# Kernel tuning notes

Measured on AMD Instinct MI355X. Metric: run time of the kernel, lower is better.

## Reference

```python
import jax, jax.numpy as jnp
import numpy as np

ALPHA = 0.2  # LeakyReLU negative slope
N = 1024     # num_particles
DIM = 3
F_IN = 2 * DIM   # 6
NH = 64          # n_hidden_features
H = 4            # n_heads
T = 12


def _gat_attend(feat, a_vec, slope):
    # feat: (..., N, K); a_vec: (..., 2K) split into source/dest halves
    k = feat.shape[-1]
    f_src = jnp.einsum('...nk,...k->...n', feat, a_vec[..., :k])
    f_dst = jnp.einsum('...nk,...k->...n', feat, a_vec[..., k:])
    e = jax.nn.leaky_relu(f_src[..., :, None] + f_dst[..., None, :], slope)
    attn = jax.nn.softmax(e, axis=-1)  # (..., N, N) dense particle attention
    return jnp.einsum('...ij,...jk->...ik', attn, feat)


def pat_layer(x, W_heads, a_heads, W_out, a_out):
    # x: (N, F_IN); W_heads: (H, F_IN, NH); a_heads: (H, 2*NH)
    # W_out: (H*NH, F_OUT); a_out: (2*F_OUT)
    hW = jnp.einsum('nf,hfk->hnk', x, W_heads)          # (H, N, NH)
    heads = jax.nn.elu(_gat_attend(hW, a_heads, ALPHA))  # (H, N, NH)
    x2 = heads.transpose(1, 0, 2).reshape(x.shape[0], -1)  # (N, H*NH) concat
    hW2 = x2 @ W_out                                     # (N, F_OUT)
    return _gat_attend(hW2, a_out, ALPHA)                # output head, no elu


def setup_inputs() -> dict:
    key = jax.random.key(0)
    ks = jax.random.split(key, 13)
    s = 0.1
    d = {'states': jax.random.normal(ks[0], (T, N, F_IN), jnp.float32)}
    names = ['Wx', 'ax', 'Wxo', 'axo', 'Wh', 'ah', 'Who', 'aho', 'Wy', 'ay', 'Wyo', 'ayo']
    shapes = [(H, F_IN, NH), (H, 2 * NH), (H * NH, F_IN), (2 * F_IN)] * 3
    for i, (nm, sh) in enumerate(zip(names, shapes)):
        sh = sh if isinstance(sh, tuple) else (sh,)
        d[nm] = s * jax.random.normal(ks[i + 1], sh, jnp.float32)
    return d


def reference(states, Wx, ax, Wxo, axo, Wh, ah, Who, aho, Wy, ay, Wyo, ayo):
    def step(h_prev, x_t):
        h_t = pat_layer(x_t, Wx, ax, Wxo, axo) + pat_layer(h_prev, Wh, ah, Who, aho)
        y_t = x_t + pat_layer(h_t, Wy, ay, Wyo, ayo)
        return h_t, y_t

    h0 = jnp.zeros((N, F_IN), states.dtype)
    _, ys = jax.lax.scan(step, h0, states)
    return ys  # (T, N, 2*dim)
```

## Files before the change

### kernel.cpp

```cpp
#include <hip/hip_runtime.h>
#include <hip/hip_bf16.h>

#define ALPHA 0.2f

typedef float v2f __attribute__((ext_vector_type(2)));
typedef short bf16x8 __attribute__((ext_vector_type(8)));
typedef float f32x4 __attribute__((ext_vector_type(4)));

__device__ __forceinline__ float wsum(float v){
  #pragma unroll
  for (int m = 1; m < 64; m <<= 1) v += __shfl_xor(v, m, 64);
  return v;
}
__device__ __forceinline__ float wmax(float v){
  #pragma unroll
  for (int m = 1; m < 64; m <<= 1) v = fmaxf(v, __shfl_xor(v, m, 64));
  return v;
}

__global__ void k_detect(const unsigned short* __restrict__ s, int n, int* __restrict__ flag){
  int i = blockIdx.x * 256 + threadIdx.x;
  if (i < n){
    unsigned short u = s[i];
    if ((u & 0x7F80u) == 0x7F80u) atomicOr(flag, 1);
  }
}

struct Ptr13 { const void* p[13]; };
__global__ void k_cvtAll(Ptr13 src, float* __restrict__ xs, float* __restrict__ wsW,
                         const int* __restrict__ flag){
  const int n = blockIdx.x * 256 + threadIdx.x;
  const int F = *flag;
  if (n < 73728){
    xs[n] = F ? ((const float*)src.p[0])[n]
              : __bfloat162float(((const __hip_bfloat16*)src.p[0])[n]);
    return;
  }
  const int m = n - 73728;
  if (m >= 10788) return;
  const int segend[12] = {1536,2048,3584,3596,5132,5644,7180,7192,8728,9240,10776,10788};
  const int dstoff[12] = {0,1536,2048,3584,3600,5136,5648,7184,7200,8736,9248,10784};
  int seg = 0;
  #pragma unroll
  for (int i = 0; i < 12; ++i) if (m >= segend[i]) seg = i + 1;
  const int local = m - (seg ? segend[seg - 1] : 0);
  float v;
  if (F) v = ((const float*)src.p[seg + 1])[local];
  else   v = __bfloat162float(((const __hip_bfloat16*)src.p[seg + 1])[local]);
  wsW[dstoff[seg] + local] = v;
}

__launch_bounds__(256)
__global__ void k_prepT(const float* __restrict__ X, const float* __restrict__ W,
                        const float* __restrict__ a,
                        __hip_bfloat16* __restrict__ Vt, float* __restrict__ fsd)
{
  __shared__ float WS[384];
  __shared__ float aS[128];
  __shared__ __align__(16) __hip_bfloat16 tileT[64 * 264];
  const int t = threadIdx.x;
  const int b = blockIdx.y;
  const int h = blockIdx.z;
  const int row0 = blockIdx.x * 256;
  const int row = row0 + t;
  for (int i = t; i < 384; i += 256) WS[i] = W[h * 384 + i];
  if (t < 128) aS[t] = a[h * 128 + t];
  __syncthreads();
  float x[6];
  const float* xp = X + ((size_t)b * 1024 + row) * 6;
  #pragma unroll
  for (int f = 0; f < 6; ++f) x[f] = xp[f];
  float fs = 0.f, fd = 0.f;
  for (int k = 0; k < 64; ++k){
    float v = 0.f;
    #pragma unroll
    for (int f = 0; f < 6; ++f) v += x[f] * WS[f * 64 + k];
    fs += v * aS[k]; fd += v * aS[64 + k];
    tileT[k * 264 + t] = __float2bfloat16(v);
  }
  fsd[(((size_t)b * 4 + h) * 2 + 0) * 1024 + row] = fs;
  fsd[(((size_t)b * 4 + h) * 2 + 1) * 1024 + row] = fd;
  __syncthreads();
  const int k = t >> 2, seg = t & 3;
  __hip_bfloat16* dst = Vt + (((size_t)b * 4 + h) * 64 + k) * 1032 + row0 + seg * 64;
  const __hip_bfloat16* src = tileT + k * 264 + seg * 64;
  #pragma unroll
  for (int i = 0; i < 8; ++i)
    ((uint4*)dst)[i] = ((const uint4*)src)[i];
}

__launch_bounds__(256)
__global__ void k_attM(const __hip_bfloat16* __restrict__ Vt, const float* __restrict__ fsd,
                       const float* __restrict__ Wout, const float* __restrict__ aout,
                       float* __restrict__ hW2part, float* __restrict__ f2part)
{
  const int h = blockIdx.x & 3;
  const int row0 = (blockIdx.x >> 2) * 64;
  const int b = blockIdx.y;
  const int t = threadIdx.x;
  const int wv = t >> 6, lane = t & 63;
  const int n = lane & 15, q = lane >> 4;
  const size_t bh = (size_t)b * 4 + h;

  __shared__ float dS[1024];
  __shared__ float WoS[384];
  __shared__ float aoS[12];
  __shared__ float redW[4];

  const float* fb = fsd + bh * 2048;
  float4 dv = *(const float4*)(fb + 1024 + t * 4);
  for (int i = t; i < 384; i += 256) WoS[i] = Wout[h * 384 + i];
  if (t < 12) aoS[t] = aout[t];
  *(float4*)&dS[t * 4] = dv;
  const float sW = fb[row0 + wv * 16 + n];
  float lm = fmaxf(fmaxf(dv.x, dv.y), fmaxf(dv.z, dv.w));
  lm = wmax(lm);
  if (lane == 0) redW[wv] = lm;
  __syncthreads();
  const float maxd = fmaxf(fmaxf(redW[0], redW[1]), fmaxf(redW[2], redW[3]));
  float mW = sW + maxd; mW = fmaxf(mW, ALPHA * mW);

  const __hip_bfloat16* vbase = Vt + (bh * 64 + n) * 1032 + q * 8;
  f32x4 acc[4];
  #pragma unroll
  for (int nt = 0; nt < 4; ++nt) acc[nt] = (f32x4){0.f, 0.f, 0.f, 0.f};
  float den = 0.f;

  for (int jt = 0; jt < 16; ++jt){
    bf16x8 b0[4], b1[4];
    #pragma unroll
    for (int nt = 0; nt < 4; ++nt){
      b0[nt] = *(const bf16x8*)(vbase + nt * 16512 + jt * 64);
      b1[nt] = *(const bf16x8*)(vbase + nt * 16512 + jt * 64 + 32);
    }
    const float* dp = &dS[jt * 64 + q * 8];
    float d0[8], d1[8];
    *(float4*)&d0[0] = *(const float4*)(dp);
    *(float4*)&d0[4] = *(const float4*)(dp + 4);
    *(float4*)&d1[0] = *(const float4*)(dp + 32);
    *(float4*)&d1[4] = *(const float4*)(dp + 36);
    bf16x8 a0, a1;
    #pragma unroll
    for (int i = 0; i < 8; ++i){
      float e0 = sW + d0[i]; e0 = fmaxf(e0, ALPHA * e0);
      __hip_bfloat16 w0 = __float2bfloat16(__expf(fminf(e0 - mW, 0.f)));
      a0[i] = __builtin_bit_cast(short, w0);
      den += __bfloat162float(w0);
      float e1 = sW + d1[i]; e1 = fmaxf(e1, ALPHA * e1);
      __hip_bfloat16 w1 = __float2bfloat16(__expf(fminf(e1 - mW, 0.f)));
      a1[i] = __builtin_bit_cast(short, w1);
      den += __bfloat162float(w1);
    }
    #pragma unroll
    for (int nt = 0; nt < 4; ++nt)
      acc[nt] = __builtin_amdgcn_mfma_f32_16x16x32_bf16(a0, b0[nt], acc[nt], 0, 0, 0);
    #pragma unroll
    for (int nt = 0; nt < 4; ++nt)
      acc[nt] = __builtin_amdgcn_mfma_f32_16x16x32_bf16(a1, b1[nt], acc[nt], 0, 0, 0);
  }
  den += __shfl_xor(den, 16, 64);
  den += __shfl_xor(den, 32, 64);

  float o[4][6];
  #pragma unroll
  for (int reg = 0; reg < 4; ++reg)
    #pragma unroll
    for (int f = 0; f < 6; ++f) o[reg][f] = 0.f;
  #pragma unroll
  for (int reg = 0; reg < 4; ++reg){
    const float dn = __shfl(den, q * 4 + reg, 64);
    #pragma unroll
    for (int nt = 0; nt < 4; ++nt){
      float v = acc[nt][reg] / dn;
      v = v > 0.f ? v : (__expf(v) - 1.f);
      #pragma unroll
      for (int f = 0; f < 6; ++f) o[reg][f] += v * WoS[(nt * 16 + n) * 6 + f];
    }
  }
  #pragma unroll
  for (int mm = 1; mm < 16; mm <<= 1)
    #pragma unroll
    for (int reg = 0; reg < 4; ++reg)
      #pragma unroll
      for (int f = 0; f < 6; ++f) o[reg][f] += __shfl_xor(o[reg][f], mm, 64);
  if (n == 0){
    #pragma unroll
    for (int reg = 0; reg < 4; ++reg){
      const int row = row0 + wv * 16 + q * 4 + reg;
      float* hp = hW2part + bh * 6144 + row * 6;
      float fs = 0.f, fd = 0.f;
      #pragma unroll
      for (int f = 0; f < 6; ++f){
        hp[f] = o[reg][f];
        fs += o[reg][f] * aoS[f]; fd += o[reg][f] * aoS[6 + f];
      }
      f2part[bh * 2048 + row]        = fs;
      f2part[bh * 2048 + 1024 + row] = fd;
    }
  }
}

__launch_bounds__(256)
__global__ void k_attP(const __hip_bfloat16* __restrict__ VtP, const float* __restrict__ fsd,
                       const float* __restrict__ Wout, const float* __restrict__ aout,
                       float* __restrict__ hW2part, float* __restrict__ f2part)
{
  const int h = blockIdx.x & 3;
  const int row0 = (blockIdx.x >> 2) * 16;
  const int t = threadIdx.x;
  const int wv = t >> 6, lane = t & 63;
  const int n = lane & 15, q = lane >> 4;

  __shared__ float dS[1024];
  __shared__ float WoS[384];
  __shared__ float aoS[12];
  __shared__ float redW[4];
  __shared__ float accS[4][16][65];
  __shared__ float denP[4][16];

  const float* fb = fsd + (size_t)h * 2048;
  float4 dv = *(const float4*)(fb + 1024 + t * 4);
  for (int i = t; i < 384; i += 256) WoS[i] = Wout[h * 384 + i];
  if (t < 12) aoS[t] = aout[t];
  *(float4*)&dS[t * 4] = dv;
  const float sW = fb[row0 + n];
  float lm = fmaxf(fmaxf(dv.x, dv.y), fmaxf(dv.z, dv.w));
  lm = wmax(lm);
  if (lane == 0) redW[wv] = lm;
  __syncthreads();
  const float maxd = fmaxf(fmaxf(redW[0], redW[1]), fmaxf(redW[2], redW[3]));
  float mW = sW + maxd; mW = fmaxf(mW, ALPHA * mW);

  const __hip_bfloat16* vbase = VtP + ((size_t)h * 64 + n) * 1024 + q * 8;
  f32x4 acc[4];
  #pragma unroll
  for (int nt = 0; nt < 4; ++nt) acc[nt] = (f32x4){0.f, 0.f, 0.f, 0.f};
  float den = 0.f;

  #pragma unroll
  for (int u = 0; u < 4; ++u){
    const int jt = wv * 4 + u;
    bf16x8 b0[4], b1[4];
    #pragma unroll
    for (int nt = 0; nt < 4; ++nt){
      b0[nt] = *(const bf16x8*)(vbase + nt * 16384 + jt * 64);
      b1[nt] = *(const bf16x8*)(vbase + nt * 16384 + jt * 64 + 32);
    }
    const float* dp = &dS[jt * 64 + q * 8];
    float d0[8], d1[8];
    *(float4*)&d0[0] = *(const float4*)(dp);
    *(float4*)&d0[4] = *(const float4*)(dp + 4);
    *(float4*)&d1[0] = *(const float4*)(dp + 32);
    *(float4*)&d1[4] = *(const float4*)(dp + 36);
    bf16x8 a0, a1;
    #pragma unroll
    for (int i = 0; i < 8; ++i){
      float e0 = sW + d0[i]; e0 = fmaxf(e0, ALPHA * e0);
      __hip_bfloat16 w0 = __float2bfloat16(__expf(fminf(e0 - mW, 0.f)));
      a0[i] = __builtin_bit_cast(short, w0);
      den += __bfloat162float(w0);
      float e1 = sW + d1[i]; e1 = fmaxf(e1, ALPHA * e1);
      __hip_bfloat16 w1 = __float2bfloat16(__expf(fminf(e1 - mW, 0.f)));
      a1[i] = __builtin_bit_cast(short, w1);
      den += __bfloat162float(w1);
    }
    #pragma unroll
    for (int nt = 0; nt < 4; ++nt)
      acc[nt] = __builtin_amdgcn_mfma_f32_16x16x32_bf16(a0, b0[nt], acc[nt], 0, 0, 0);
    #pragma unroll
    for (int nt = 0; nt < 4; ++nt)
      acc[nt] = __builtin_amdgcn_mfma_f32_16x16x32_bf16(a1, b1[nt], acc[nt], 0, 0, 0);
  }
  den += __shfl_xor(den, 16, 64);
  den += __shfl_xor(den, 32, 64);
  if (lane < 16) denP[wv][lane] = den;
  #pragma unroll
  for (int nt = 0; nt < 4; ++nt)
    #pragma unroll
    for (int reg = 0; reg < 4; ++reg)
      accS[wv][q * 4 + reg][nt * 16 + n] = acc[nt][reg];
  __syncthreads();

  const int r = t >> 4, kq = t & 15;
  const float dn = denP[0][r] + denP[1][r] + denP[2][r] + denP[3][r];
  float o[6] = {0.f,0.f,0.f,0.f,0.f,0.f};
  #pragma unroll
  for (int j4 = 0; j4 < 4; ++j4){
    const int k = kq * 4 + j4;
    float v = (accS[0][r][k] + accS[1][r][k] + accS[2][r][k] + accS[3][r][k]) / dn;
    v = v > 0.f ? v : (__expf(v) - 1.f);
    #pragma unroll
    for (int f = 0; f < 6; ++f) o[f] += v * WoS[k * 6 + f];
  }
  #pragma unroll
  for (int mm = 1; mm < 16; mm <<= 1)
    #pragma unroll
    for (int f = 0; f < 6; ++f) o[f] += __shfl_xor(o[f], mm, 64);
  if (kq == 0){
    const int row = row0 + r;
    float* hp = hW2part + (size_t)h * 6144 + row * 6;
    float fs = 0.f, fd = 0.f;
    #pragma unroll
    for (int f = 0; f < 6; ++f){
      hp[f] = o[f];
      fs += o[f] * aoS[f]; fd += o[f] * aoS[6 + f];
    }
    f2part[(size_t)h * 2048 + row]        = fs;
    f2part[(size_t)h * 2048 + 1024 + row] = fd;
  }
}

__launch_bounds__(256)
__global__ void k_attB(const float* __restrict__ hW2part, const float* __restrict__ f2part,
                       const float* __restrict__ Lx_t, float* __restrict__ h_t,
                       const float* __restrict__ Wh, const float* __restrict__ ah,
                       __hip_bfloat16* __restrict__ hWn, float* __restrict__ fn)
{
  const int t = threadIdx.x;
  const int row0 = blockIdx.x * 4;
  const int wv = t >> 6, lane = t & 63;
  __shared__ float featS[6144];
  __shared__ float dS[1024];
  __shared__ float sS[4];
  __shared__ float redW[4];
  __shared__ float htS[4][6];
  __shared__ float WnS[1536];
  __shared__ float anS[512];

  for (int i = t; i < 6144; i += 256)
    featS[i] = hW2part[i] + hW2part[6144 + i] + hW2part[12288 + i] + hW2part[18432 + i];
  for (int i = t; i < 1024; i += 256)
    dS[i] = f2part[1024 + i] + f2part[3072 + i] + f2part[5120 + i] + f2part[7168 + i];
  if (t < 4){
    const int r = row0 + t;
    sS[t] = f2part[r] + f2part[2048 + r] + f2part[4096 + r] + f2part[6144 + r];
  }
  for (int i = t; i < 1536; i += 256) WnS[i] = Wh[i];
  for (int i = t; i < 512;  i += 256) anS[i] = ah[i];
  __syncthreads();
  float lm = -1.0e30f;
  for (int i = t; i < 1024; i += 256) lm = fmaxf(lm, dS[i]);
  lm = wmax(lm);
  if (lane == 0) redW[wv] = lm;
  __syncthreads();
  const float maxd = fmaxf(fmaxf(redW[0], redW[1]), fmaxf(redW[2], redW[3]));
  {
    const int r = wv, row = row0 + r;
    const float s = sS[r];
    float m = s + maxd; m = m > 0.f ? m : ALPHA * m;
    float num[6] = {0.f,0.f,0.f,0.f,0.f,0.f};
    float den = 0.f;
    for (int j = lane; j < 1024; j += 64){
      float e = s + dS[j]; e = e > 0.f ? e : ALPHA * e;
      float w = __expf(fminf(e - m, 0.f));
      den += w;
      const float* fr = &featS[j * 6];
      #pragma unroll
      for (int f = 0; f < 6; ++f) num[f] += w * fr[f];
    }
    den = wsum(den);
    #pragma unroll
    for (int f = 0; f < 6; ++f) num[f] = wsum(num[f]);
    if (lane == 0){
      #pragma unroll
      for (int f = 0; f < 6; ++f){
        float hv = Lx_t[row * 6 + f] + num[f] / den;
        h_t[row * 6 + f] = hv;
        htS[r][f] = hv;
      }
    }
  }
  __syncthreads();
  {
    const int k = lane, rw = row0 + wv;
    float hv[6];
    #pragma unroll
    for (int f = 0; f < 6; ++f) hv[f] = htS[wv][f];
    #pragma unroll
    for (int h = 0; h < 4; ++h){
      float acc = 0.f;
      #pragma unroll
      for (int f = 0; f < 6; ++f) acc += hv[f] * WnS[(h * 6 + f) * 64 + k];
      hWn[((size_t)h * 64 + k) * 1024 + rw] = __float2bfloat16(acc);
      float ps = wsum(acc * anS[h * 128 + k]);
      float pd = wsum(acc * anS[h * 128 + 64 + k]);
      if (k == 0){
        fn[((size_t)h * 2 + 0) * 1024 + rw] = ps;
        fn[((size_t)h * 2 + 1) * 1024 + rw] = pd;
      }
    }
  }
}

template<int MODE>
__launch_bounds__(256)
__global__ void k_attO(const float* __restrict__ hW2part, const float* __restrict__ f2part,
                       const float* __restrict__ addsrc, float* __restrict__ outf,
                       void* __restrict__ outv, int outOff, const int* __restrict__ flag)
{
  const int b = blockIdx.y;
  const int row0 = blockIdx.x * 16;
  const int t = threadIdx.x;
  const int wv = t >> 6, lane = t & 63;
  __shared__ float featS[6144];
  __shared__ float dS[1024];
  __shared__ float sS[16];
  __shared__ float redW[4];

  const float* hp = hW2part + (size_t)b * 24576;
  for (int i = t; i < 6144; i += 256)
    featS[i] = hp[i] + hp[6144 + i] + hp[12288 + i] + hp[18432 + i];
  const float* fp = f2part + (size_t)b * 8192;
  for (int i = t; i < 1024; i += 256)
    dS[i] = fp[1024 + i] + fp[3072 + i] + fp[5120 + i] + fp[7168 + i];
  if (t < 16){
    const int r = row0 + t;
    sS[t] = fp[r] + fp[2048 + r] + fp[4096 + r] + fp[6144 + r];
  }
  __syncthreads();
  float lm = -1.0e30f;
  for (int i = t; i < 1024; i += 256) lm = fmaxf(lm, dS[i]);
  lm = wmax(lm);
  if (lane == 0) redW[wv] = lm;
  __syncthreads();
  const float maxd = fmaxf(fmaxf(redW[0], redW[1]), fmaxf(redW[2], redW[3]));

  const int r = t >> 4, jq = t & 15;
  const int row = row0 + r;
  const float s = sS[r];
  float m = s + maxd; m = m > 0.f ? m : ALPHA * m;
  float num[6] = {0.f,0.f,0.f,0.f,0.f,0.f};
  float den = 0.f;
  for (int j = jq; j < 1024; j += 16){
    float e = s + dS[j]; e = e > 0.f ? e : ALPHA * e;
    float w = __expf(fminf(e - m, 0.f));
    den += w;
    const float* fr = &featS[j * 6];
    #pragma unroll
    for (int f = 0; f < 6; ++f) num[f] += w * fr[f];
  }
  #pragma unroll
  for (int mm = 1; mm < 16; mm <<= 1){
    den += __shfl_xor(den, mm, 64);
    #pragma unroll
    for (int f = 0; f < 6; ++f) num[f] += __shfl_xor(num[f], mm, 64);
  }

  if (jq == 0){
    if (MODE == 0){
      float* dst = outf + ((size_t)b * 1024 + row) * 6;
      #pragma unroll
      for (int f = 0; f < 6; ++f) dst[f] = num[f] / den;
    } else {
      const float* xsrc = addsrc + ((size_t)b * 1024 + row) * 6;
      const int base = outOff + b * 6144 + row * 6;
      if (*flag){
        float* dst = (float*)outv;
        #pragma unroll
        for (int f = 0; f < 6; ++f) dst[base + f] = xsrc[f] + num[f] / den;
      } else {
        __hip_bfloat16* dst = (__hip_bfloat16*)outv;
        #pragma unroll
        for (int f = 0; f < 6; ++f) dst[base + f] = __float2bfloat16(xsrc[f] + num[f] / den);
      }
    }
  }
}

extern "C" void kernel_launch(void* const* d_in, const int* in_sizes, int n_in,
                              void* d_out, int out_size, void* d_ws, size_t ws_size,
                              hipStream_t stream) {
  (void)in_sizes; (void)n_in; (void)out_size;

  const size_t avail = ws_size / 4;
  int CH = 0;
  const int cands[6] = {12, 6, 4, 3, 2, 1};
  for (int i = 0; i < 6; ++i){
    if (232000u + (size_t)cands[i] * 303104u <= avail){ CH = cands[i]; break; }
  }
  if (CH == 0) return;

  float* ws = (float*)d_ws;
  size_t off = 0;
  int*   flag = (int*)(ws + off); off += 16;
  float* xs   = ws + off; off += 73728;
  float* wsW  = ws + off; off += 10800;
  float* Lx    = ws + off; off += 73728;
  float* h_all = ws + off; off += 73728;
  float* p2hW2 = ws + off; off += (size_t)CH * 24576;
  float* p2f2  = ws + off; off += (size_t)CH * 8192;
  float* hWc   = ws + off; off += (size_t)CH * 262144;
  float* fc    = ws + off; off += (size_t)CH * 8192;

  hipMemsetAsync(flag, 0, 4, stream);
  k_detect<<<288, 256, 0, stream>>>((const unsigned short*)d_in[0], 73728, flag);
  Ptr13 ptrs;
  for (int i = 0; i < 13; ++i) ptrs.p[i] = d_in[i];
  k_cvtAll<<<331, 256, 0, stream>>>(ptrs, xs, wsW, flag);

  const int dstoff[12] = {0,1536,2048,3584,3600,5136,5648,7184,7200,8736,9248,10784};
  float *Wx = wsW + dstoff[0], *ax = wsW + dstoff[1], *Wxo = wsW + dstoff[2], *axo = wsW + dstoff[3];
  float *Wh = wsW + dstoff[4], *ah = wsW + dstoff[5], *Who = wsW + dstoff[6], *aho = wsW + dstoff[7];
  float *Wy = wsW + dstoff[8], *ay = wsW + dstoff[9], *Wyo = wsW + dstoff[10], *ayo = wsW + dstoff[11];

  __hip_bfloat16* VtG = (__hip_bfloat16*)hWc;

  for (int t0 = 0; t0 < 12; t0 += CH){
    k_prepT<<<dim3(4, CH, 4), 256, 0, stream>>>(xs + (size_t)t0 * 6144, Wx, ax, VtG, fc);
    k_attM<<<dim3(64, CH), 256, 0, stream>>>(VtG, fc, Wxo, axo, p2hW2, p2f2);
    k_attO<0><<<dim3(64, CH), 256, 0, stream>>>(p2hW2, p2f2, nullptr, Lx + (size_t)t0 * 6144,
                                                nullptr, 0, flag);
  }

  __hip_bfloat16* VtP = (__hip_bfloat16*)hWc;
  float* fh = fc;
  hipMemsetAsync(VtP, 0, 4 * 64 * 1024 * sizeof(__hip_bfloat16), stream);
  hipMemsetAsync(fh,  0, 8192 * sizeof(float), stream);
  for (int t = 0; t < 12; ++t){
    k_attP<<<dim3(256, 1), 256, 0, stream>>>(VtP, fh, Who, aho, p2hW2, p2f2);
    k_attB<<<256, 256, 0, stream>>>(p2hW2, p2f2, Lx + (size_t)t * 6144,
                                    h_all + (size_t)t * 6144, Wh, ah, VtP, fh);
  }

  for (int t0 = 0; t0 < 12; t0 += CH){
    k_prepT<<<dim3(4, CH, 4), 256, 0, stream>>>(h_all + (size_t)t0 * 6144, Wy, ay, VtG, fc);
    k_attM<<<dim3(64, CH), 256, 0, stream>>>(VtG, fc, Wyo, ayo, p2hW2, p2f2);
    k_attO<2><<<dim3(64, CH), 256, 0, stream>>>(p2hW2, p2f2, xs + (size_t)t0 * 6144, nullptr,
                                                d_out, t0 * 6144, flag);
  }
}
```

Before: 417.5 us.

## Reassociate head attention to attend on raw 6-dim inputs before projecting

Uses linearity: attention over hW = xW equals (attention over x)·W, and the attention logits become x·(W a), so each head attends over 6-dim inputs instead of 64-dim features. This replaces the bf16 MFMA attention over 64-wide V tiles, the transposed V precompute, and the per-head partial buffers with one fused kernel that computes the scores, the 6-wide weighted sums, the projection, ELU and the output projection. It also precomputes W·a per layer and restructures the recurrence into two kernels per step. The risk is that the scalar 6-wide inner loops lose MFMA throughput, but the arithmetic is far smaller and it also avoids the bf16 rounding of V.

```diff
diff --git a/kernel.cpp b/kernel.cpp
--- a/kernel.cpp
+++ b/kernel.cpp
@@ -3,15 +3,6 @@
 
 #define ALPHA 0.2f
 
-typedef float v2f __attribute__((ext_vector_type(2)));
-typedef short bf16x8 __attribute__((ext_vector_type(8)));
-typedef float f32x4 __attribute__((ext_vector_type(4)));
-
-__device__ __forceinline__ float wsum(float v){
-  #pragma unroll
-  for (int m = 1; m < 64; m <<= 1) v += __shfl_xor(v, m, 64);
-  return v;
-}
 __device__ __forceinline__ float wmax(float v){
   #pragma unroll
   for (int m = 1; m < 64; m <<= 1) v = fmaxf(v, __shfl_xor(v, m, 64));
@@ -50,293 +41,194 @@
   wsW[dstoff[seg] + local] = v;
 }
 
+__global__ void k_prew(const float* __restrict__ wsW, float* __restrict__ WaG,
+                       float* __restrict__ h0)
+{
+  if (blockIdx.x == 1){
+    for (int i = threadIdx.x; i < 6144; i += 256) h0[i] = 0.f;
+    return;
+  }
+  if (threadIdx.x < 144){
+    const int d = threadIdx.x;
+    const int L = d / 48, r2 = d % 48, h = r2 / 12, sd = (r2 % 12) / 6, f = r2 % 6;
+    const int Woff[3] = {0, 3600, 7200};
+    const int aoff[3] = {1536, 5136, 8736};
+    float s = 0.f;
+    for (int k = 0; k < 64; ++k)
+      s += wsW[Woff[L] + h * 384 + f * 64 + k] * wsW[aoff[L] + h * 128 + sd * 64 + k];
+    WaG[((L * 4 + h) * 2 + sd) * 8 + f] = s;
+  }
+}
+
+template<int LPR>
 __launch_bounds__(256)
-__global__ void k_prepT(const float* __restrict__ X, const float* __restrict__ W,
-                        const float* __restrict__ a,
-                        __hip_bfloat16* __restrict__ Vt, float* __restrict__ fsd)
+__global__ void k_gatA(const float* __restrict__ X, const float* __restrict__ Wa,
+                       const float* __restrict__ W64, const float* __restrict__ Wout,
+                       const float* __restrict__ aout,
+                       float* __restrict__ y6out, float* __restrict__ fsdout)
 {
-  __shared__ float WS[384];
-  __shared__ float aS[128];
-  __shared__ __align__(16) __hip_bfloat16 tileT[64 * 264];
-  const int t = threadIdx.x;
-  const int b = blockIdx.y;
-  const int h = blockIdx.z;
-  const int row0 = blockIdx.x * 256;
-  const int row = row0 + t;
-  for (int i = t; i < 384; i += 256) WS[i] = W[h * 384 + i];
-  if (t < 128) aS[t] = a[h * 128 + t];
-  __syncthreads();
-  float x[6];
-  const float* xp = X + ((size_t)b * 1024 + row) * 6;
+  constexpr int R   = 256 / LPR;
+  constexpr int LPP = 64 / R;
+  constexpr int KPT = 64 / LPP;
+  const int t  = threadIdx.x;
+  const int tb = blockIdx.y;
+  const int row0 = blockIdx.x * R;
+
+  __shared__ float xS[1024 * 7];
+  __shared__ float dT[1024 * 5];
+  __shared__ float WS[1536];
+  __shared__ float WoS[1536];
+  __shared__ float WaS[64];
+  __shared__ float aoS[12];
+  __shared__ float sS[4 * R];
+  __shared__ float maxdS[4];
+  __shared__ float hS[R][4][8];
+  __shared__ float ypS[R][4][8];
+  __shared__ float yS[R][6];
+
+  const float* Xt = X + (size_t)tb * 6144;
+  {
+    const float4* x4 = (const float4*)Xt;
+    for (int i = t; i < 1536; i += 256){
+      float4 v = x4[i];
+      const int base = i * 4;
+      xS[(base    ) / 6 * 7 + (base    ) % 6] = v.x;
+      xS[(base + 1) / 6 * 7 + (base + 1) % 6] = v.y;
+      xS[(base + 2) / 6 * 7 + (base + 2) % 6] = v.z;
+      xS[(base + 3) / 6 * 7 + (base + 3) % 6] = v.w;
+    }
+  }
+  for (int i = t; i < 1536; i += 256){ WS[i] = W64[i]; WoS[i] = Wout[i]; }
+  if (t < 64) WaS[t] = Wa[t];
+  if (t < 12) aoS[t] = aout[t];
+  __syncthreads();
+
+  for (int p = t; p < 4096; p += 256){
+    const int j = p >> 2, h = p & 3;
+    const float* xr = &xS[j * 7];
+    const float* wa = &WaS[(h * 2 + 1) * 8];
+    float s = 0.f;
+    #pragma unroll
+    for (int f = 0; f < 6; ++f) s += xr[f] * wa[f];
+    dT[j * 5 + h] = s;
+  }
+  if (t < 4 * R){
+    const int r = t >> 2, h = t & 3;
+    const float* xr = &xS[(row0 + r) * 7];
+    const float* wa = &WaS[(h * 2) * 8];
+    float s = 0.f;
+    #pragma unroll
+    for (int f = 0; f < 6; ++f) s += xr[f] * wa[f];
+    sS[h * R + r] = s;
+  }
+  __syncthreads();
+  {
+    const int h = t >> 6, lane = t & 63;
+    float lm = -1.0e30f;
+    for (int j = lane; j < 1024; j += 64) lm = fmaxf(lm, dT[j * 5 + h]);
+    lm = wmax(lm);
+    if (lane == 0) maxdS[h] = lm;
+  }
+  __syncthreads();
+
+  const int r = t / LPR, jg = t % LPR;
   #pragma unroll
-  for (int f = 0; f < 6; ++f) x[f] = xp[f];
-  float fs = 0.f, fd = 0.f;
-  for (int k = 0; k < 64; ++k){
-    float v = 0.f;
-    #pragma unroll
-    for (int f = 0; f < 6; ++f) v += x[f] * WS[f * 64 + k];
-    fs += v * aS[k]; fd += v * aS[64 + k];
-    tileT[k * 264 + t] = __float2bfloat16(v);
-  }
-  fsd[(((size_t)b * 4 + h) * 2 + 0) * 1024 + row] = fs;
-  fsd[(((size_t)b * 4 + h) * 2 + 1) * 1024 + row] = fd;
-  __syncthreads();
-  const int k = t >> 2, seg = t & 3;
-  __hip_bfloat16* dst = Vt + (((size_t)b * 4 + h) * 64 + k) * 1032 + row0 + seg * 64;
-  const __hip_bfloat16* src = tileT + k * 264 + seg * 64;
-  #pragma unroll
-  for (int i = 0; i < 8; ++i)
-    ((uint4*)dst)[i] = ((const uint4*)src)[i];
-}
-
+  for (int h = 0; h < 4; ++h){
+    const float s = sS[h * R + r];
+    float sm = s + maxdS[h];
+    const float m = fmaxf(sm, ALPHA * sm);
+    float acc[6] = {0.f,0.f,0.f,0.f,0.f,0.f};
+    float den = 0.f;
+    for (int j = jg; j < 1024; j += LPR){
+      float e = s + dT[j * 5 + h]; e = fmaxf(e, ALPHA * e);
+      const float w = __expf(fminf(e - m, 0.f));
+      den += w;
+      const float* xr = &xS[j * 7];
+      #pragma unroll
+      for (int f = 0; f < 6; ++f) acc[f] += w * xr[f];
+    }
+    #pragma unroll
+    for (int mm = 1; mm < LPR; mm <<= 1){
+      den += __shfl_xor(den, mm, 64);
+      #pragma unroll
+      for (int f = 0; f < 6; ++f) acc[f] += __shfl_xor(acc[f], mm, 64);
+    }
+    if (jg == 0){
+      hS[r][h][0] = den;
+      #pragma unroll
+      for (int f = 0; f < 6; ++f) hS[r][h][1 + f] = acc[f];
+    }
+  }
+  __syncthreads();
+
+  {
+    const int p = t / LPP, kq = t % LPP;
+    const int pr = p >> 2, ph = p & 3;
+    const float inv = 1.f / hS[pr][ph][0];
+    float hv[6];
+    #pragma unroll
+    for (int f = 0; f < 6; ++f) hv[f] = hS[pr][ph][1 + f] * inv;
+    float yp[6] = {0.f,0.f,0.f,0.f,0.f,0.f};
+    #pragma unroll
+    for (int kk = 0; kk < KPT; ++kk){
+      const int k = kq * KPT + kk;
+      float o = 0.f;
+      #pragma unroll
+      for (int f = 0; f < 6; ++f) o += hv[f] * WS[ph * 384 + f * 64 + k];
+      o = o > 0.f ? o : (__expf(o) - 1.f);
+      const float* wo = &WoS[(ph * 64 + k) * 6];
+      #pragma unroll
+      for (int f = 0; f < 6; ++f) yp[f] += o * wo[f];
+    }
+    #pragma unroll
+    for (int mm = 1; mm < LPP; mm <<= 1)
+      #pragma unroll
+      for (int f = 0; f < 6; ++f) yp[f] += __shfl_xor(yp[f], mm, 64);
+    if (kq == 0){
+      #pragma unroll
+      for (int f = 0; f < 6; ++f) ypS[pr][ph][f] = yp[f];
+    }
+  }
+  __syncthreads();
+  if (t < R * 6){
+    const int rr = t / 6, f = t % 6;
+    const float y = ypS[rr][0][f] + ypS[rr][1][f] + ypS[rr][2][f] + ypS[rr][3][f];
+    yS[rr][f] = y;
+    y6out[(size_t)tb * 6144 + (row0 + rr) * 6 + f] = y;
+  }
+  __syncthreads();
+  if (t < 2 * R){
+    const int rr = t >> 1, sd = t & 1;
+    float s = 0.f;
+    #pragma unroll
+    for (int f = 0; f < 6; ++f) s += yS[rr][f] * aoS[sd * 6 + f];
+    fsdout[(size_t)tb * 2048 + sd * 1024 + row0 + rr] = s;
+  }
+}
+
+template<int MODE>
 __launch_bounds__(256)
-__global__ void k_attM(const __hip_bfloat16* __restrict__ Vt, const float* __restrict__ fsd,
-                       const float* __restrict__ Wout, const float* __restrict__ aout,
-                       float* __restrict__ hW2part, float* __restrict__ f2part)
+__global__ void k_gatB(const float* __restrict__ y6, const float* __restrict__ fsd,
+                       const float* __restrict__ addsrc, float* __restrict__ f32out,
+                       void* __restrict__ outv, const int* __restrict__ flag)
 {
-  const int h = blockIdx.x & 3;
-  const int row0 = (blockIdx.x >> 2) * 64;
-  const int b = blockIdx.y;
+  const int tb = blockIdx.y;
+  const int row0 = blockIdx.x * 16;
   const int t = threadIdx.x;
   const int wv = t >> 6, lane = t & 63;
-  const int n = lane & 15, q = lane >> 4;
-  const size_t bh = (size_t)b * 4 + h;
-
-  __shared__ float dS[1024];
-  __shared__ float WoS[384];
-  __shared__ float aoS[12];
+  __shared__ __align__(16) float featS[6144];
+  __shared__ __align__(16) float dS[1024];
+  __shared__ float sS[16];
   __shared__ float redW[4];
 
-  const float* fb = fsd + bh * 2048;
-  float4 dv = *(const float4*)(fb + 1024 + t * 4);
-  for (int i = t; i < 384; i += 256) WoS[i] = Wout[h * 384 + i];
-  if (t < 12) aoS[t] = aout[t];
-  *(float4*)&dS[t * 4] = dv;
-  const float sW = fb[row0 + wv * 16 + n];
-  float lm = fmaxf(fmaxf(dv.x, dv.y), fmaxf(dv.z, dv.w));
-  lm = wmax(lm);
-  if (lane == 0) redW[wv] = lm;
-  __syncthreads();
-  const float maxd = fmaxf(fmaxf(redW[0], redW[1]), fmaxf(redW[2], redW[3]));
-  float mW = sW + maxd; mW = fmaxf(mW, ALPHA * mW);
-
-  const __hip_bfloat16* vbase = Vt + (bh * 64 + n) * 1032 + q * 8;
-  f32x4 acc[4];
-  #pragma unroll
-  for (int nt = 0; nt < 4; ++nt) acc[nt] = (f32x4){0.f, 0.f, 0.f, 0.f};
-  float den = 0.f;
-
-  for (int jt = 0; jt < 16; ++jt){
-    bf16x8 b0[4], b1[4];
-    #pragma unroll
-    for (int nt = 0; nt < 4; ++nt){
-      b0[nt] = *(const bf16x8*)(vbase + nt * 16512 + jt * 64);
-      b1[nt] = *(const bf16x8*)(vbase + nt * 16512 + jt * 64 + 32);
-    }
-    const float* dp = &dS[jt * 64 + q * 8];
-    float d0[8], d1[8];
-    *(float4*)&d0[0] = *(const float4*)(dp);
-    *(float4*)&d0[4] = *(const float4*)(dp + 4);
-    *(float4*)&d1[0] = *(const float4*)(dp + 32);
-    *(float4*)&d1[4] = *(const float4*)(dp + 36);
-    bf16x8 a0, a1;
-    #pragma unroll
-    for (int i = 0; i < 8; ++i){
-      float e0 = sW + d0[i]; e0 = fmaxf(e0, ALPHA * e0);
-      __hip_bfloat16 w0 = __float2bfloat16(__expf(fminf(e0 - mW, 0.f)));
-      a0[i] = __builtin_bit_cast(short, w0);
-      den += __bfloat162float(w0);
-      float e1 = sW + d1[i]; e1 = fmaxf(e1, ALPHA * e1);
-      __hip_bfloat16 w1 = __float2bfloat16(__expf(fminf(e1 - mW, 0.f)));
-      a1[i] = __builtin_bit_cast(short, w1);
-      den += __bfloat162float(w1);
-    }
-    #pragma unroll
-    for (int nt = 0; nt < 4; ++nt)
-      acc[nt] = __builtin_amdgcn_mfma_f32_16x16x32_bf16(a0, b0[nt], acc[nt], 0, 0, 0);
-    #pragma unroll
-    for (int nt = 0; nt < 4; ++nt)
-      acc[nt] = __builtin_amdgcn_mfma_f32_16x16x32_bf16(a1, b1[nt], acc[nt], 0, 0, 0);
-  }
-  den += __shfl_xor(den, 16, 64);
-  den += __shfl_xor(den, 32, 64);
-
-  float o[4][6];
-  #pragma unroll
-  for (int reg = 0; reg < 4; ++reg)
-    #pragma unroll
-    for (int f = 0; f < 6; ++f) o[reg][f] = 0.f;
-  #pragma unroll
-  for (int reg = 0; reg < 4; ++reg){
-    const float dn = __shfl(den, q * 4 + reg, 64);
-    #pragma unroll
-    for (int nt = 0; nt < 4; ++nt){
-      float v = acc[nt][reg] / dn;
-      v = v > 0.f ? v : (__expf(v) - 1.f);
-      #pragma unroll
-      for (int f = 0; f < 6; ++f) o[reg][f] += v * WoS[(nt * 16 + n) * 6 + f];
-    }
-  }
-  #pragma unroll
-  for (int mm = 1; mm < 16; mm <<= 1)
-    #pragma unroll
-    for (int reg = 0; reg < 4; ++reg)
-      #pragma unroll
-      for (int f = 0; f < 6; ++f) o[reg][f] += __shfl_xor(o[reg][f], mm, 64);
-  if (n == 0){
-    #pragma unroll
-    for (int reg = 0; reg < 4; ++reg){
-      const int row = row0 + wv * 16 + q * 4 + reg;
-      float* hp = hW2part + bh * 6144 + row * 6;
-      float fs = 0.f, fd = 0.f;
-      #pragma unroll
-      for (int f = 0; f < 6; ++f){
-        hp[f] = o[reg][f];
-        fs += o[reg][f] * aoS[f]; fd += o[reg][f] * aoS[6 + f];
-      }
-      f2part[bh * 2048 + row]        = fs;
-      f2part[bh * 2048 + 1024 + row] = fd;
-    }
-  }
-}
-
-__launch_bounds__(256)
-__global__ void k_attP(const __hip_bfloat16* __restrict__ VtP, const float* __restrict__ fsd,
-                       const float* __restrict__ Wout, const float* __restrict__ aout,
-                       float* __restrict__ hW2part, float* __restrict__ f2part)
-{
-  const int h = blockIdx.x & 3;
-  const int row0 = (blockIdx.x >> 2) * 16;
-  const int t = threadIdx.x;
-  const int wv = t >> 6, lane = t & 63;
-  const int n = lane & 15, q = lane >> 4;
-
-  __shared__ float dS[1024];
-  __shared__ float WoS[384];
-  __shared__ float aoS[12];
-  __shared__ float redW[4];
-  __shared__ float accS[4][16][65];
-  __shared__ float denP[4][16];
-
-  const float* fb = fsd + (size_t)h * 2048;
-  float4 dv = *(const float4*)(fb + 1024 + t * 4);
-  for (int i = t; i < 384; i += 256) WoS[i] = Wout[h * 384 + i];
-  if (t < 12) aoS[t] = aout[t];
-  *(float4*)&dS[t * 4] = dv;
-  const float sW = fb[row0 + n];
-  float lm = fmaxf(fmaxf(dv.x, dv.y), fmaxf(dv.z, dv.w));
-  lm = wmax(lm);
-  if (lane == 0) redW[wv] = lm;
-  __syncthreads();
-  const float maxd = fmaxf(fmaxf(redW[0], redW[1]), fmaxf(redW[2], redW[3]));
-  float mW = sW + maxd; mW = fmaxf(mW, ALPHA * mW);
-
-  const __hip_bfloat16* vbase = VtP + ((size_t)h * 64 + n) * 1024 + q * 8;
-  f32x4 acc[4];
-  #pragma unroll
-  for (int nt = 0; nt < 4; ++nt) acc[nt] = (f32x4){0.f, 0.f, 0.f, 0.f};
-  float den = 0.f;
-
-  #pragma unroll
-  for (int u = 0; u < 4; ++u){
-    const int jt = wv * 4 + u;
-    bf16x8 b0[4], b1[4];
-    #pragma unroll
-    for (int nt = 0; nt < 4; ++nt){
-      b0[nt] = *(const bf16x8*)(vbase + nt * 16384 + jt * 64);
-      b1[nt] = *(const bf16x8*)(vbase + nt * 16384 + jt * 64 + 32);
-    }
-    const float* dp = &dS[jt * 64 + q * 8];
-    float d0[8], d1[8];
-    *(float4*)&d0[0] = *(const float4*)(dp);
-    *(float4*)&d0[4] = *(const float4*)(dp + 4);
-    *(float4*)&d1[0] = *(const float4*)(dp + 32);
-    *(float4*)&d1[4] = *(const float4*)(dp + 36);
-    bf16x8 a0, a1;
-    #pragma unroll
-    for (int i = 0; i < 8; ++i){
-      float e0 = sW + d0[i]; e0 = fmaxf(e0, ALPHA * e0);
-      __hip_bfloat16 w0 = __float2bfloat16(__expf(fminf(e0 - mW, 0.f)));
-      a0[i] = __builtin_bit_cast(short, w0);
-      den += __bfloat162float(w0);
-      float e1 = sW + d1[i]; e1 = fmaxf(e1, ALPHA * e1);
-      __hip_bfloat16 w1 = __float2bfloat16(__expf(fminf(e1 - mW, 0.f)));
-      a1[i] = __builtin_bit_cast(short, w1);
-      den += __bfloat162float(w1);
-    }
-    #pragma unroll
-    for (int nt = 0; nt < 4; ++nt)
-      acc[nt] = __builtin_amdgcn_mfma_f32_16x16x32_bf16(a0, b0[nt], acc[nt], 0, 0, 0);
-    #pragma unroll
-    for (int nt = 0; nt < 4; ++nt)
-      acc[nt] = __builtin_amdgcn_mfma_f32_16x16x32_bf16(a1, b1[nt], acc[nt], 0, 0, 0);
-  }
-  den += __shfl_xor(den, 16, 64);
-  den += __shfl_xor(den, 32, 64);
-  if (lane < 16) denP[wv][lane] = den;
-  #pragma unroll
-  for (int nt = 0; nt < 4; ++nt)
-    #pragma unroll
-    for (int reg = 0; reg < 4; ++reg)
-      accS[wv][q * 4 + reg][nt * 16 + n] = acc[nt][reg];
-  __syncthreads();
-
-  const int r = t >> 4, kq = t & 15;
-  const float dn = denP[0][r] + denP[1][r] + denP[2][r] + denP[3][r];
-  float o[6] = {0.f,0.f,0.f,0.f,0.f,0.f};
-  #pragma unroll
-  for (int j4 = 0; j4 < 4; ++j4){
-    const int k = kq * 4 + j4;
-    float v = (accS[0][r][k] + accS[1][r][k] + accS[2][r][k] + accS[3][r][k]) / dn;
-    v = v > 0.f ? v : (__expf(v) - 1.f);
-    #pragma unroll
-    for (int f = 0; f < 6; ++f) o[f] += v * WoS[k * 6 + f];
-  }
-  #pragma unroll
-  for (int mm = 1; mm < 16; mm <<= 1)
-    #pragma unroll
-    for (int f = 0; f < 6; ++f) o[f] += __shfl_xor(o[f], mm, 64);
-  if (kq == 0){
-    const int row = row0 + r;
-    float* hp = hW2part + (size_t)h * 6144 + row * 6;
-    float fs = 0.f, fd = 0.f;
-    #pragma unroll
-    for (int f = 0; f < 6; ++f){
-      hp[f] = o[f];
-      fs += o[f] * aoS[f]; fd += o[f] * aoS[6 + f];
-    }
-    f2part[(size_t)h * 2048 + row]        = fs;
-    f2part[(size_t)h * 2048 + 1024 + row] = fd;
-  }
-}
-
-__launch_bounds__(256)
-__global__ void k_attB(const float* __restrict__ hW2part, const float* __restrict__ f2part,
-                       const float* __restrict__ Lx_t, float* __restrict__ h_t,
-                       const float* __restrict__ Wh, const float* __restrict__ ah,
-                       __hip_bfloat16* __restrict__ hWn, float* __restrict__ fn)
-{
-  const int t = threadIdx.x;
-  const int row0 = blockIdx.x * 4;
-  const int wv = t >> 6, lane = t & 63;
-  __shared__ float featS[6144];
-  __shared__ float dS[1024];
-  __shared__ float sS[4];
-  __shared__ float redW[4];
-  __shared__ float htS[4][6];
-  __shared__ float WnS[1536];
-  __shared__ float anS[512];
-
-  for (int i = t; i < 6144; i += 256)
-    featS[i] = hW2part[i] + hW2part[6144 + i] + hW2part[12288 + i] + hW2part[18432 + i];
-  for (int i = t; i < 1024; i += 256)
-    dS[i] = f2part[1024 + i] + f2part[3072 + i] + f2part[5120 + i] + f2part[7168 + i];
-  if (t < 4){
-    const int r = row0 + t;
-    sS[t] = f2part[r] + f2part[2048 + r] + f2part[4096 + r] + f2part[6144 + r];
-  }
-  for (int i = t; i < 1536; i += 256) WnS[i] = Wh[i];
-  for (int i = t; i < 512;  i += 256) anS[i] = ah[i];
+  const float* y6t = y6 + (size_t)tb * 6144;
+  const float* ft  = fsd + (size_t)tb * 2048;
+  {
+    const float4* h4 = (const float4*)y6t;
+    for (int i = t; i < 1536; i += 256) *(float4*)&featS[i * 4] = h4[i];
+    if (t < 256) *(float4*)&dS[t * 4] = ((const float4*)(ft + 1024))[t];
+    if (t < 16) sS[t] = ft[row0 + t];
+  }
   __syncthreads();
   float lm = -1.0e30f;
   for (int i = t; i < 1024; i += 256) lm = fmaxf(lm, dS[i]);
@@ -344,96 +236,16 @@
   if (lane == 0) redW[wv] = lm;
   __syncthreads();
   const float maxd = fmaxf(fmaxf(redW[0], redW[1]), fmaxf(redW[2], redW[3]));
-  {
-    const int r = wv, row = row0 + r;
-    const float s = sS[r];
-    float m = s + maxd; m = m > 0.f ? m : ALPHA * m;
-    float num[6] = {0.f,0.f,0.f,0.f,0.f,0.f};
-    float den = 0.f;
-    for (int j = lane; j < 1024; j += 64){
-      float e = s + dS[j]; e = e > 0.f ? e : ALPHA * e;
-      float w = __expf(fminf(e - m, 0.f));
-      den += w;
-      const float* fr = &featS[j * 6];
-      #pragma unroll
-      for (int f = 0; f < 6; ++f) num[f] += w * fr[f];
-    }
-    den = wsum(den);
-    #pragma unroll
-    for (int f = 0; f < 6; ++f) num[f] = wsum(num[f]);
-    if (lane == 0){
-      #pragma unroll
-      for (int f = 0; f < 6; ++f){
-        float hv = Lx_t[row * 6 + f] + num[f] / den;
-        h_t[row * 6 + f] = hv;
-        htS[r][f] = hv;
-      }
-    }
-  }
-  __syncthreads();
-  {
-    const int k = lane, rw = row0 + wv;
-    float hv[6];
-    #pragma unroll
-    for (int f = 0; f < 6; ++f) hv[f] = htS[wv][f];
-    #pragma unroll
-    for (int h = 0; h < 4; ++h){
-      float acc = 0.f;
-      #pragma unroll
-      for (int f = 0; f < 6; ++f) acc += hv[f] * WnS[(h * 6 + f) * 64 + k];
-      hWn[((size_t)h * 64 + k) * 1024 + rw] = __float2bfloat16(acc);
-      float ps = wsum(acc * anS[h * 128 + k]);
-      float pd = wsum(acc * anS[h * 128 + 64 + k]);
-      if (k == 0){
-        fn[((size_t)h * 2 + 0) * 1024 + rw] = ps;
-        fn[((size_t)h * 2 + 1) * 1024 + rw] = pd;
-      }
-    }
-  }
-}
-
-template<int MODE>
-__launch_bounds__(256)
-__global__ void k_attO(const float* __restrict__ hW2part, const float* __restrict__ f2part,
-                       const float* __restrict__ addsrc, float* __restrict__ outf,
-                       void* __restrict__ outv, int outOff, const int* __restrict__ flag)
-{
-  const int b = blockIdx.y;
-  const int row0 = blockIdx.x * 16;
-  const int t = threadIdx.x;
-  const int wv = t >> 6, lane = t & 63;
-  __shared__ float featS[6144];
-  __shared__ float dS[1024];
-  __shared__ float sS[16];
-  __shared__ float redW[4];
-
-  const float* hp = hW2part + (size_t)b * 24576;
-  for (int i = t; i < 6144; i += 256)
-    featS[i] = hp[i] + hp[6144 + i] + hp[12288 + i] + hp[18432 + i];
-  const float* fp = f2part + (size_t)b * 8192;
-  for (int i = t; i < 1024; i += 256)
-    dS[i] = fp[1024 + i] + fp[3072 + i] + fp[5120 + i] + fp[7168 + i];
-  if (t < 16){
-    const int r = row0 + t;
-    sS[t] = fp[r] + fp[2048 + r] + fp[4096 + r] + fp[6144 + r];
-  }
-  __syncthreads();
-  float lm = -1.0e30f;
-  for (int i = t; i < 1024; i += 256) lm = fmaxf(lm, dS[i]);
-  lm = wmax(lm);
-  if (lane == 0) redW[wv] = lm;
-  __syncthreads();
-  const float maxd = fmaxf(fmaxf(redW[0], redW[1]), fmaxf(redW[2], redW[3]));
 
   const int r = t >> 4, jq = t & 15;
   const int row = row0 + r;
   const float s = sS[r];
-  float m = s + maxd; m = m > 0.f ? m : ALPHA * m;
+  float m = s + maxd; m = fmaxf(m, ALPHA * m);
   float num[6] = {0.f,0.f,0.f,0.f,0.f,0.f};
   float den = 0.f;
   for (int j = jq; j < 1024; j += 16){
-    float e = s + dS[j]; e = e > 0.f ? e : ALPHA * e;
-    float w = __expf(fminf(e - m, 0.f));
+    float e = s + dS[j]; e = fmaxf(e, ALPHA * e);
+    const float w = __expf(fminf(e - m, 0.f));
     den += w;
     const float* fr = &featS[j * 6];
     #pragma unroll
@@ -445,23 +257,28 @@
     #pragma unroll
     for (int f = 0; f < 6; ++f) num[f] += __shfl_xor(num[f], mm, 64);
   }
-
   if (jq == 0){
+    const float inv = 1.f / den;
     if (MODE == 0){
-      float* dst = outf + ((size_t)b * 1024 + row) * 6;
-      #pragma unroll
-      for (int f = 0; f < 6; ++f) dst[f] = num[f] / den;
+      float* dst = f32out + (size_t)tb * 6144 + row * 6;
+      #pragma unroll
+      for (int f = 0; f < 6; ++f) dst[f] = num[f] * inv;
+    } else if (MODE == 1){
+      const float* a = addsrc + row * 6;
+      float* dst = f32out + row * 6;
+      #pragma unroll
+      for (int f = 0; f < 6; ++f) dst[f] = a[f] + num[f] * inv;
     } else {
-      const float* xsrc = addsrc + ((size_t)b * 1024 + row) * 6;
-      const int base = outOff + b * 6144 + row * 6;
+      const float* a = addsrc + (size_t)tb * 6144 + row * 6;
+      const int base = tb * 6144 + row * 6;
       if (*flag){
         float* dst = (float*)outv;
         #pragma unroll
-        for (int f = 0; f < 6; ++f) dst[base + f] = xsrc[f] + num[f] / den;
+        for (int f = 0; f < 6; ++f) dst[base + f] = a[f] + num[f] * inv;
       } else {
         __hip_bfloat16* dst = (__hip_bfloat16*)outv;
         #pragma unroll
-        for (int f = 0; f < 6; ++f) dst[base + f] = __float2bfloat16(xsrc[f] + num[f] / den);
+        for (int f = 0; f < 6; ++f) dst[base + f] = __float2bfloat16(a[f] + num[f] * inv);
       }
     }
   }
@@ -473,59 +290,42 @@
   (void)in_sizes; (void)n_in; (void)out_size;
 
   const size_t avail = ws_size / 4;
-  int CH = 0;
-  const int cands[6] = {12, 6, 4, 3, 2, 1};
-  for (int i = 0; i < 6; ++i){
-    if (232000u + (size_t)cands[i] * 303104u <= avail){ CH = cands[i]; break; }
-  }
-  if (CH == 0) return;
+  if (avail < 340000u) return;
 
   float* ws = (float*)d_ws;
   size_t off = 0;
-  int*   flag = (int*)(ws + off); off += 16;
-  float* xs   = ws + off; off += 73728;
-  float* wsW  = ws + off; off += 10800;
+  int*   flag  = (int*)(ws + off); off += 16;
+  float* xs    = ws + off; off += 73728;
+  float* wsW   = ws + off; off += 10800;
   float* Lx    = ws + off; off += 73728;
-  float* h_all = ws + off; off += 73728;
-  float* p2hW2 = ws + off; off += (size_t)CH * 24576;
-  float* p2f2  = ws + off; off += (size_t)CH * 8192;
-  float* hWc   = ws + off; off += (size_t)CH * 262144;
-  float* fc    = ws + off; off += (size_t)CH * 8192;
+  float* WaG   = ws + off; off += 256;
+  float* h_all = ws + off; off += 79872;
+  float* y6a   = ws + off; off += 73728;
+  float* fsdA  = ws + off; off += 24576;
 
   hipMemsetAsync(flag, 0, 4, stream);
   k_detect<<<288, 256, 0, stream>>>((const unsigned short*)d_in[0], 73728, flag);
   Ptr13 ptrs;
   for (int i = 0; i < 13; ++i) ptrs.p[i] = d_in[i];
   k_cvtAll<<<331, 256, 0, stream>>>(ptrs, xs, wsW, flag);
-
-  const int dstoff[12] = {0,1536,2048,3584,3600,5136,5648,7184,7200,8736,9248,10784};
-  float *Wx = wsW + dstoff[0], *ax = wsW + dstoff[1], *Wxo = wsW + dstoff[2], *axo = wsW + dstoff[3];
-  float *Wh = wsW + dstoff[4], *ah = wsW + dstoff[5], *Who = wsW + dstoff[6], *aho = wsW + dstoff[7];
-  float *Wy = wsW + dstoff[8], *ay = wsW + dstoff[9], *Wyo = wsW + dstoff[10], *ayo = wsW + dstoff[11];
-
-  __hip_bfloat16* VtG = (__hip_bfloat16*)hWc;
-
-  for (int t0 = 0; t0 < 12; t0 += CH){
-    k_prepT<<<dim3(4, CH, 4), 256, 0, stream>>>(xs + (size_t)t0 * 6144, Wx, ax, VtG, fc);
-    k_attM<<<dim3(64, CH), 256, 0, stream>>>(VtG, fc, Wxo, axo, p2hW2, p2f2);
-    k_attO<0><<<dim3(64, CH), 256, 0, stream>>>(p2hW2, p2f2, nullptr, Lx + (size_t)t0 * 6144,
-                                                nullptr, 0, flag);
-  }
-
-  __hip_bfloat16* VtP = (__hip_bfloat16*)hWc;
-  float* fh = fc;
-  hipMemsetAsync(VtP, 0, 4 * 64 * 1024 * sizeof(__hip_bfloat16), stream);
-  hipMemsetAsync(fh,  0, 8192 * sizeof(float), stream);
+  k_prew<<<2, 256, 0, stream>>>(wsW, WaG, h_all);
+
+  float *Wx = wsW, *Wxo = wsW + 2048, *axo = wsW + 3584;
+  float *Wh = wsW + 3600, *Who = wsW + 5648, *aho = wsW + 7184;
+  float *Wy = wsW + 7200, *Wyo = wsW + 9248, *ayo = wsW + 10784;
+
+  k_gatA<16><<<dim3(64, 12), 256, 0, stream>>>(xs, WaG, Wx, Wxo, axo, y6a, fsdA);
+  k_gatB<0><<<dim3(64, 12), 256, 0, stream>>>(y6a, fsdA, nullptr, Lx, nullptr, flag);
+
   for (int t = 0; t < 12; ++t){
-    k_attP<<<dim3(256, 1), 256, 0, stream>>>(VtP, fh, Who, aho, p2hW2, p2f2);
-    k_attB<<<256, 256, 0, stream>>>(p2hW2, p2f2, Lx + (size_t)t * 6144,
-                                    h_all + (size_t)t * 6144, Wh, ah, VtP, fh);
-  }
-
-  for (int t0 = 0; t0 < 12; t0 += CH){
-    k_prepT<<<dim3(4, CH, 4), 256, 0, stream>>>(h_all + (size_t)t0 * 6144, Wy, ay, VtG, fc);
-    k_attM<<<dim3(64, CH), 256, 0, stream>>>(VtG, fc, Wyo, ayo, p2hW2, p2f2);
-    k_attO<2><<<dim3(64, CH), 256, 0, stream>>>(p2hW2, p2f2, xs + (size_t)t0 * 6144, nullptr,
-                                                d_out, t0 * 6144, flag);
-  }
-}
+    k_gatA<64><<<dim3(256, 1), 256, 0, stream>>>(h_all + (size_t)t * 6144, WaG + 64,
+                                                 Wh, Who, aho, y6a, fsdA);
+    k_gatB<1><<<dim3(64, 1), 256, 0, stream>>>(y6a, fsdA, Lx + (size_t)t * 6144,
+                                               h_all + (size_t)(t + 1) * 6144,
+                                               nullptr, flag);
+  }
+
+  k_gatA<16><<<dim3(64, 12), 256, 0, stream>>>(h_all + 6144, WaG + 128, Wy, Wyo, ayo,
+                                               y6a, fsdA);
+  k_gatB<2><<<dim3(64, 12), 256, 0, stream>>>(y6a, fsdA, xs, nullptr, d_out, flag);
+}
```

New measurement: 541.2 us. 29.6% more time.
